# Kernel tuning notes

Measured on AMD Instinct MI355X. Metric: run time of the kernel, lower is better.

The kernel has to match this reference:

```python
import jax, jax.numpy as jnp
import numpy as np

N = 100000      # nodes
E = 1600000     # edges (before self-loops)
F_IN = 128      # dataset.num_features
H1 = 128        # hidden_channels/2
H2 = 256        # hidden_channels
C = 40          # dataset.num_classes
EPS = 1e-5      # BatchNorm eps
NEG_SLOPE = 0.2 # GATConv leaky_relu slope


def setup_inputs() -> dict:
    key = jax.random.key(0)
    ks = jax.random.split(key, 12)
    p = lambda k, shape: jax.random.normal(k, shape, jnp.float32) * 0.1
    x = jax.random.normal(ks[0], (N, F_IN), jnp.float32)
    edge_index = jax.random.randint(ks[1], (2, E), 0, N, dtype=jnp.int64)
    return dict(
        x=x, edge_index=edge_index,
        w1=p(ks[2], (F_IN, H1)), as1=p(ks[3], (H1,)), ad1=p(ks[4], (H1,)), b1=jnp.zeros(H1, jnp.float32),
        g1=jnp.ones(H1, jnp.float32), be1=jnp.zeros(H1, jnp.float32), rm1=jnp.zeros(H1, jnp.float32), rv1=jnp.ones(H1, jnp.float32),
        w2=p(ks[5], (H1, H2)), as2=p(ks[6], (H2,)), ad2=p(ks[7], (H2,)), b2=jnp.zeros(H2, jnp.float32),
        g2=jnp.ones(H2, jnp.float32), be2=jnp.zeros(H2, jnp.float32), rm2=jnp.zeros(H2, jnp.float32), rv2=jnp.ones(H2, jnp.float32),
        w3=p(ks[8], (H2, C)), as3=p(ks[9], (C,)), ad3=p(ks[10], (C,)), b3=jnp.zeros(C, jnp.float32),
    )


def gat_conv(x, src, dst, W, a_src, a_dst, b):
    """PyG GATConv (heads=1, add_self_loops already applied to src/dst)."""
    h = x @ W                                  # [N, F_out]
    alpha_src = h @ a_src                      # [N]
    alpha_dst = h @ a_dst                      # [N]
    logits = jax.nn.leaky_relu(alpha_src[src] + alpha_dst[dst], NEG_SLOPE)  # [E']
    # segment softmax over incoming edges of each dst node
    m = jax.ops.segment_max(logits, dst, num_segments=N)
    e = jnp.exp(logits - m[dst])
    denom = jax.ops.segment_sum(e, dst, num_segments=N)
    alpha = e / denom[dst]                     # [E']
    out = jax.ops.segment_sum(h[src] * alpha[:, None], dst, num_segments=N)
    return out + b


def bn_eval(x, gamma, beta, mean, var):
    return (x - mean) * jax.lax.rsqrt(var + EPS) * gamma + beta


def reference(x, edge_index,
              w1, as1, ad1, b1, g1, be1, rm1, rv1,
              w2, as2, ad2, b2, g2, be2, rm2, rv2,
              w3, as3, ad3, b3):
    # add self-loops once (PyG GATConv default add_self_loops=True)
    loop = jnp.arange(N, dtype=edge_index.dtype)
    src = jnp.concatenate([edge_index[0], loop])
    dst = jnp.concatenate([edge_index[1], loop])
    # eval mode: dropout is identity, BN uses running stats
    h = gat_conv(x, src, dst, w1, as1, ad1, b1)
    h = jnp.tanh(bn_eval(h, g1, be1, rm1, rv1))
    h = gat_conv(h, src, dst, w2, as2, ad2, b2)
    h = jnp.tanh(bn_eval(h, g2, be2, rm2, rv2))
    return gat_conv(h, src, dst, w3, as3, ad3, b3)
```

## Files before the change

### kernel.cpp

```cpp
#include <hip/hip_runtime.h>
#include <hip/hip_bf16.h>
#include <cstddef>

#define N_NODES 100000
#define E_EDGES 1600000
#define TOT_EDGES (E_EDGES + N_NODES)
#define NEG_SLOPE 0.2f
#define BN_EPS 1e-5f
#define NBKT ((N_NODES + 255) / 256)
#define NBA 512

typedef __attribute__((ext_vector_type(8))) short short8;
typedef __attribute__((ext_vector_type(4))) float f32x4;
typedef __attribute__((ext_vector_type(2))) float f32x2;
typedef __attribute__((ext_vector_type(4))) int int32x4;
typedef __attribute__((ext_vector_type(2))) int int32x2;

#if defined(__has_builtin)
#if __has_builtin(__builtin_amdgcn_make_buffer_rsrc) && __has_builtin(__builtin_amdgcn_raw_buffer_load_b128)
#define HAVE_BUFRSRC 1
#endif
#if __has_builtin(__builtin_amdgcn_make_buffer_rsrc) && __has_builtin(__builtin_amdgcn_raw_buffer_load_b64)
#define HAVE_BUF64 1
#endif
#endif

__device__ __forceinline__ unsigned short f2bf(float f) {
    union { float f; unsigned u; } c; c.f = f;
    unsigned u = c.u;
    u += 0x7fffu + ((u >> 16) & 1u);
    return (unsigned short)(u >> 16);
}
__device__ __forceinline__ float bf2f(unsigned short h) {
    union { unsigned u; float f; } c; c.u = ((unsigned)h) << 16;
    return c.f;
}
__device__ __forceinline__ unsigned short f2h(float f) {
    union { _Float16 h; unsigned short u; } c; c.h = (_Float16)f; return c.u;
}
__device__ __forceinline__ float lrelu(float t) {
    return (t > 0.f) ? t : NEG_SLOPE * t;
}
__device__ __forceinline__ float tanh_fast(float x) {
    float e = __expf(2.f * x);
    return 1.f - 2.f / (e + 1.f);
}
__device__ __forceinline__ unsigned short pk_fp8(float a, float b) {
    unsigned v;
    asm volatile("v_cvt_pk_fp8_f32 %0, %1, %2" : "=v"(v) : "v"(a), "v"(b));
    return (unsigned short)v;
}
__device__ __forceinline__ f32x2 unpk_fp8(unsigned u) {
    f32x2 r;
    asm volatile("v_cvt_pk_f32_fp8 %0, %1" : "=v"(r) : "v"(u));
    return r;
}

__device__ __forceinline__ float wave_sum63(float x) {
    x += __int_as_float(__builtin_amdgcn_update_dpp(0, __float_as_int(x), 0x111, 0xf, 0xf, true));
    x += __int_as_float(__builtin_amdgcn_update_dpp(0, __float_as_int(x), 0x112, 0xf, 0xf, true));
    x += __int_as_float(__builtin_amdgcn_update_dpp(0, __float_as_int(x), 0x114, 0xf, 0xf, true));
    x += __int_as_float(__builtin_amdgcn_update_dpp(0, __float_as_int(x), 0x118, 0xf, 0xf, true));
    x += __int_as_float(__builtin_amdgcn_update_dpp(0, __float_as_int(x), 0x142, 0xf, 0xf, true));
    x += __int_as_float(__builtin_amdgcn_update_dpp(0, __float_as_int(x), 0x143, 0xf, 0xf, true));
    return x;
}
__device__ __forceinline__ float wave_sum_bcast(float x) {
    return __int_as_float(__builtin_amdgcn_readlane(__float_as_int(wave_sum63(x)), 63));
}


__global__ __launch_bounds__(256) void csr_hist(const int* __restrict__ ei,
                                                int* __restrict__ bh) {
    __shared__ int h[NBKT];
    int t = threadIdx.x;
    for (int b = t; b < NBKT; b += 256) h[b] = 0;
    __syncthreads();
    int idx = blockIdx.x * 256 + t;
    const int stride = NBA * 256;
    for (int e = idx; e < TOT_EDGES; e += stride) {
        int d = (e < E_EDGES) ? ei[E_EDGES + e] : (e - E_EDGES);
        atomicAdd(&h[((unsigned)d) >> 8], 1);
    }
    __syncthreads();
    for (int b = t; b < NBKT; b += 256) bh[blockIdx.x * NBKT + b] = h[b];
}

__global__ __launch_bounds__(512) void csr_scan_blocks(int* __restrict__ bh,
                                                       int* __restrict__ totals) {
    __shared__ int s[NBA];
    int t = threadIdx.x, bin = blockIdx.x;
    int v = bh[t * NBKT + bin];
    s[t] = v;
    __syncthreads();
    for (int off = 1; off < NBA; off <<= 1) {
        int y = (t >= off) ? s[t - off] : 0;
        __syncthreads();
        s[t] += y;
        __syncthreads();
    }
    bh[t * NBKT + bin] = s[t] - v;
    if (t == NBA - 1) totals[bin] = s[t];
}

__global__ __launch_bounds__(512) void csr_scan_buckets(const int* __restrict__ totals,
                                                        int* __restrict__ starts) {
    __shared__ int s[512];
    int t = threadIdx.x;
    int v = (t < NBKT) ? totals[t] : 0;
    s[t] = v;
    __syncthreads();
    for (int off = 1; off < 512; off <<= 1) {
        int y = (t >= off) ? s[t - off] : 0;
        __syncthreads();
        s[t] += y;
        __syncthreads();
    }
    if (t < NBKT) starts[t] = s[t] - v;
    if (t == 0) starts[NBKT] = TOT_EDGES;
}

__global__ __launch_bounds__(256) void csr_scatter(const int* __restrict__ ei,
                                                   const int* __restrict__ bh,
                                                   const int* __restrict__ starts,
                                                   int* __restrict__ pairs) {
    __shared__ int wp[NBKT];
    int t = threadIdx.x;
    for (int b = t; b < NBKT; b += 256)
        wp[b] = starts[b] + bh[blockIdx.x * NBKT + b];
    __syncthreads();
    int idx = blockIdx.x * 256 + t;
    const int stride = NBA * 256;
    for (int e = idx; e < TOT_EDGES; e += stride) {
        int s, d;
        if (e < E_EDGES) { s = ei[e]; d = ei[E_EDGES + e]; }
        else             { s = e - E_EDGES; d = s; }
        int pos = atomicAdd(&wp[((unsigned)d) >> 8], 1);
        pairs[pos] = s | ((d & 255) << 20);
    }
}

__global__ __launch_bounds__(256) void csr_build(const int* __restrict__ pairs,
                                                 const int* __restrict__ starts,
                                                 int* __restrict__ row_ptr,
                                                 int* __restrict__ src_sorted) {
    __shared__ int nh[256];
    __shared__ int sc[256];
    __shared__ int wp[256];
    int k = blockIdx.x, t = threadIdx.x;
    int bs = starts[k], be = starts[k + 1];
    nh[t] = 0;
    __syncthreads();
    for (int i = bs + t; i < be; i += 256)
        atomicAdd(&nh[((unsigned)pairs[i]) >> 20], 1);
    __syncthreads();
    int v = nh[t];
    sc[t] = v;
    __syncthreads();
    for (int off = 1; off < 256; off <<= 1) {
        int y = (t >= off) ? sc[t - off] : 0;
        __syncthreads();
        sc[t] += y;
        __syncthreads();
    }
    int excl = sc[t] - v;
    int node = k * 256 + t;
    if (node <= N_NODES) row_ptr[node] = bs + excl;
    wp[t] = bs + excl;
    __syncthreads();
    for (int i = bs + t; i < be; i += 256) {
        unsigned p = (unsigned)pairs[i];
        int pos = atomicAdd(&wp[p >> 20], 1);
        src_sorted[pos] = (int)(p & 0xFFFFFu);
    }
}

__global__ __launch_bounds__(256) void wprep_all(
    const float* __restrict__ w1, const float* __restrict__ w2, const float* __restrict__ w3,
    const float* __restrict__ as1, const float* __restrict__ ad1,
    const float* __restrict__ as2, const float* __restrict__ ad2,
    const float* __restrict__ as3, const float* __restrict__ ad3,
    unsigned short* __restrict__ w1th, unsigned short* __restrict__ w1tl,
    unsigned short* __restrict__ w2th, unsigned short* __restrict__ w2tl,
    unsigned short* __restrict__ w3th, unsigned short* __restrict__ w3tl,
    unsigned short* __restrict__ ab1h, unsigned short* __restrict__ ab1l,
    unsigned short* __restrict__ ab3h, unsigned short* __restrict__ ab3l,
    float* __restrict__ ws2f, float* __restrict__ wd2f) {
    const int T1 = 128 * 128, T2 = 256 * 128, T3 = 48 * 256;
    const int W = T1 + T2 + T3;
    int idx = blockIdx.x * 256 + threadIdx.x;
    if (idx < W) {
        float v; unsigned short* th; unsigned short* tl; int o;
        if (idx < T1) {
            int n = idx / 128, k = idx % 128;
            v = w1[k * 128 + n]; th = w1th; tl = w1tl; o = idx;
        } else if (idx < T1 + T2) {
            int i = idx - T1; int n = i / 128, k = i % 128;
            v = w2[k * 256 + n]; th = w2th; tl = w2tl; o = i;
        } else {
            int i = idx - T1 - T2; int n = i / 256, k = i % 256;
            v = (n < 40) ? w3[k * 40 + n] : 0.f; th = w3th; tl = w3tl; o = i;
        }
        unsigned short h = f2bf(v);
        th[o] = h;
        tl[o] = f2bf(v - bf2f(h));
        return;
    }
    int j = idx - W;
    if (j < 2048) {
        int r = j / 128, k = j % 128;
        float v = 0.f;
        if (r < 2) {
            const float* a = r ? ad1 : as1;
            const float* wr = w1 + (size_t)k * 128;
            for (int n = 0; n < 128; n++) v += wr[n] * a[n];
        }
        unsigned short h = f2bf(v);
        ab1h[j] = h; ab1l[j] = f2bf(v - bf2f(h));
    } else if (j < 2048 + 4096) {
        int i = j - 2048; int r = i / 256, k = i % 256;
        float v = 0.f;
        if (r < 2) {
            const float* a = r ? ad3 : as3;
            const float* wr = w3 + (size_t)k * 40;
            for (int n = 0; n < 40; n++) v += wr[n] * a[n];
        }
        unsigned short h = f2bf(v);
        ab3h[i] = h; ab3l[i] = f2bf(v - bf2f(h));
    } else if (j < 2048 + 4096 + 256) {
        int i = j - 2048 - 4096; int r = i / 128, k = i % 128;
        const float* a = r ? ad2 : as2;
        const float* wr = w2 + (size_t)k * 256;
        float v = 0.f;
        for (int n = 0; n < 256; n++) v += wr[n] * a[n];
        if (r == 0) ws2f[k] = v; else wd2f[k] = v;
    }
}

template<int K, int NTILES, int MWAVES, int NWAVES, int NACT, bool ASPLIT, bool ALPHA, bool BNT, bool CFRAG, bool CHALF, bool AF32>
__global__ __launch_bounds__(256) void mfma_gemm(
    const unsigned short* __restrict__ Ahi, const unsigned short* __restrict__ Alo,
    const unsigned short* __restrict__ BThi, const unsigned short* __restrict__ BTlo,
    const unsigned short* __restrict__ ABh, const unsigned short* __restrict__ ABl,
    unsigned short* __restrict__ Chi, int ldc,
    const float* __restrict__ bias, const float* __restrict__ gamma,
    const float* __restrict__ beta, const float* __restrict__ rmean,
    const float* __restrict__ rvar,
    float* __restrict__ asrc, float* __restrict__ adst, int M)
{
    int lane = threadIdx.x & 63;
    int wave = threadIdx.x >> 6;
    int quad = lane >> 4;
    int l16  = lane & 15;
    long mbase = (long)blockIdx.x * (64 * MWAVES) + (long)(wave / NWAVES) * 64;
    int n0 = ((wave % NWAVES) + blockIdx.y * NWAVES) * (NTILES * 16);
    bool aw = ((wave % NWAVES) == 0) && (blockIdx.y == 0);
    const size_t CSTRIDE = (size_t)M * 32;

    size_t roff[4];
#pragma unroll
    for (int i = 0; i < 4; i++) {
        long r = mbase + i * 16 + l16;
        if (r > M - 1) r = M - 1;
        roff[i] = AF32 ? ((size_t)r * K + (size_t)(quad * 8))
                       : ((size_t)r * 32 + (size_t)(quad * 8));
    }
    const unsigned short* bh[NTILES]; const unsigned short* bl[NTILES];
#pragma unroll
    for (int j = 0; j < NTILES; j++) {
        long n = n0 + j * 16 + l16;
        bh[j] = BThi + n * K; bl[j] = BTlo + n * K;
    }
    const unsigned short* bah = nullptr; const unsigned short* bal = nullptr;
    if constexpr (ALPHA) { bah = ABh + (size_t)l16 * K; bal = ABl + (size_t)l16 * K; }
    const int ko = quad * 8;

    f32x4 acc[4][NTILES];
    f32x4 acca[4];
#pragma unroll
    for (int i = 0; i < 4; i++) {
        acca[i] = (f32x4){0.f, 0.f, 0.f, 0.f};
#pragma unroll
        for (int j = 0; j < NTILES; j++)
            acc[i][j] = (f32x4){0.f, 0.f, 0.f, 0.f};
    }

    for (int kc = 0; kc < K / 32; kc++) {
        const int k0 = kc * 32;
        short8 vah[4], vall[4], vbh[NTILES], vbl[NTILES];
#pragma unroll
        for (int i = 0; i < 4; i++) {
            if constexpr (AF32) {
                const float* xf = (const float*)Ahi;
                const float* pa = xf + roff[i] + kc * 32;
                f32x4 va = *(const f32x4*)pa;
                f32x4 vb = *(const f32x4*)(pa + 4);
#pragma unroll
                for (int q = 0; q < 8; q++) {
                    float v = (q < 4) ? va[q] : vb[q - 4];
                    unsigned short h = f2bf(v);
                    vah[i][q] = (short)h;
                    vall[i][q] = (short)f2bf(v - bf2f(h));
                }
            } else {
                const unsigned short* Ah = Ahi + (size_t)kc * CSTRIDE;
                vah[i] = *(const short8*)(Ah + roff[i]);
                if constexpr (ASPLIT) {
                    const unsigned short* Al = Alo + (size_t)kc * CSTRIDE;
                    vall[i] = *(const short8*)(Al + roff[i]);
                }
            }
        }
#pragma unroll
        for (int j = 0; j < NTILES; j++) {
            vbh[j] = *(const short8*)(bh[j] + k0 + ko);
            vbl[j] = *(const short8*)(bl[j] + k0 + ko);
        }
#pragma unroll
        for (int i = 0; i < 4; i++)
#pragma unroll
            for (int j = 0; j < NTILES; j++) {
                acc[i][j] = __builtin_amdgcn_mfma_f32_16x16x32_bf16(vah[i], vbh[j], acc[i][j], 0, 0, 0);
                acc[i][j] = __builtin_amdgcn_mfma_f32_16x16x32_bf16(vah[i], vbl[j], acc[i][j], 0, 0, 0);
                if constexpr (ASPLIT)
                    acc[i][j] = __builtin_amdgcn_mfma_f32_16x16x32_bf16(vall[i], vbh[j], acc[i][j], 0, 0, 0);
            }
        if constexpr (ALPHA) {
            if (aw) {
                short8 vbah = *(const short8*)(bah + k0 + ko);
                short8 vbal = *(const short8*)(bal + k0 + ko);
#pragma unroll
                for (int i = 0; i < 4; i++) {
                    acca[i] = __builtin_amdgcn_mfma_f32_16x16x32_bf16(vah[i], vbah, acca[i], 0, 0, 0);
                    acca[i] = __builtin_amdgcn_mfma_f32_16x16x32_bf16(vah[i], vbal, acca[i], 0, 0, 0);
                    if constexpr (ASPLIT)
                        acca[i] = __builtin_amdgcn_mfma_f32_16x16x32_bf16(vall[i], vbah, acca[i], 0, 0, 0);
                }
            }
        }
    }

#pragma unroll
    for (int i = 0; i < 4; i++)
#pragma unroll
        for (int j = 0; j < NTILES; j++) {
            int col = n0 + j * 16 + l16;
            float bb = 0.f, rs = 1.f, gg = 1.f, bt = 0.f, rm = 0.f;
            if constexpr (BNT) {
                bb = bias[col]; gg = gamma[col]; bt = beta[col];
                rm = rmean[col]; rs = rsqrtf(rvar[col] + BN_EPS);
            }
#pragma unroll
            for (int r = 0; r < 4; r++) {
                long row = mbase + i * 16 + quad * 4 + r;
                if (row < M && col < NACT) {
                    float v = acc[i][j][r];
                    if constexpr (BNT) v = tanh_fast((v + bb - rm) * rs * gg + bt);
                    if constexpr (CFRAG) {
                        Chi[(size_t)(col >> 5) * CSTRIDE + (size_t)row * 32 + (col & 31)] = f2bf(v);
                    } else {
                        Chi[row * ldc + col] = CHALF ? f2h(v) : f2bf(v);
                    }
                }
            }
        }
    if constexpr (ALPHA) {
        if (aw) {
#pragma unroll
            for (int i = 0; i < 4; i++)
#pragma unroll
                for (int r = 0; r < 4; r++) {
                    long row = mbase + i * 16 + quad * 4 + r;
                    if (row < M) {
                        float v = acca[i][r];
                        if (l16 == 0) asrc[row] = v;
                        else if (l16 == 1) adst[row] = v;
                    }
                }
        }
    }
}

template<int MODE>
__global__ __launch_bounds__(256) void gat_agg_wide(
    const unsigned short* __restrict__ hsrc,
    const float* __restrict__ asrc, const float* __restrict__ adst,
    const int* __restrict__ row_ptr, const int* __restrict__ src_sorted,
    const float* __restrict__ bias, const float* __restrict__ gamma,
    const float* __restrict__ beta, const float* __restrict__ rmean,
    const float* __restrict__ rvar,
    const float* __restrict__ wsn, const float* __restrict__ wdn,
    unsigned short* __restrict__ ohi,
    float* __restrict__ outf,
    float* __restrict__ asrc_n, float* __restrict__ adst_n)
{
    constexpr int SH  = (MODE == 0) ? 8 : 7;
    constexpr int BPL = (MODE == 0) ? 16 : 8;
    constexpr int NF  = (MODE == 2) ? 4 : 8;

    __shared__ __align__(16) float2 esw[4][64];
    __shared__ __align__(16) float red[4][4][132];

    int wave = threadIdx.x >> 6;
    int lane = threadIdx.x & 63;
    int node = blockIdx.x * 4 + wave;
    if (node >= N_NODES) return;

    int start = row_ptr[node];
    int end = row_ptr[node + 1];
    int deg = end - start;
    float ad = adst[node];
    int sub = lane >> 4;
    int foff = (lane & 15) * BPL;
    int tpos = (lane & 3) * 16 + (lane >> 2);

#if defined(HAVE_BUFRSRC) && defined(HAVE_BUF64)
    auto rsrc = __builtin_amdgcn_make_buffer_rsrc((void*)hsrc, (short)0,
                                                  N_NODES << SH, 0x00020000);
#endif

    float acc[NF];
#pragma unroll
    for (int i = 0; i < NF; i++) acc[i] = 0.f;

    auto ld = [&](int vo) {
        if constexpr (MODE == 0) {
#if defined(HAVE_BUFRSRC) && defined(HAVE_BUF64)
            return __builtin_amdgcn_raw_buffer_load_b128(rsrc, vo, 0, 0);
#else
            return *reinterpret_cast<const int32x4*>(
                reinterpret_cast<const char*>(hsrc) + (unsigned)vo);
#endif
        } else {
#if defined(HAVE_BUFRSRC) && defined(HAVE_BUF64)
            return __builtin_amdgcn_raw_buffer_load_b64(rsrc, vo, 0, 0);
#else
            return *reinterpret_cast<const int32x2*>(
                reinterpret_cast<const char*>(hsrc) + (unsigned)vo);
#endif
        }
    };
    auto fmaN = [&](auto u, float ww) {
        if constexpr (MODE == 0) {
            union { decltype(u) v; unsigned w[4]; } c; c.v = u;
#pragma unroll
            for (int i = 0; i < 4; i++) {
                union { unsigned u; _Float16 h[2]; } t; t.u = c.w[i];
                acc[2 * i]     += ww * (float)t.h[0];
                acc[2 * i + 1] += ww * (float)t.h[1];
            }
        } else if constexpr (MODE == 1) {
            union { decltype(u) v; unsigned w[2]; } c; c.v = u;
#pragma unroll
            for (int i = 0; i < 2; i++) {
                f32x2 lo = unpk_fp8(c.w[i]);
                f32x2 hi = unpk_fp8(c.w[i] >> 16);
                acc[4 * i]     += ww * lo.x;
                acc[4 * i + 1] += ww * lo.y;
                acc[4 * i + 2] += ww * hi.x;
                acc[4 * i + 3] += ww * hi.y;
            }
        } else {
            union { decltype(u) v; unsigned w[2]; } c; c.v = u;
#pragma unroll
            for (int i = 0; i < 2; i++) {
                union { unsigned u; _Float16 h[2]; } t; t.u = c.w[i];
                acc[2 * i]     += ww * (float)t.h[0];
                acc[2 * i + 1] += ww * (float)t.h[1];
            }
        }
    };
    auto gather = [&](int nst) {
        const float2* ep = &esw[wave][sub * 16];
#pragma unroll
        for (int b = 0; b < 4; b++) {
            int s0 = b * 4;
            if (s0 < nst) {
                f32x4 p01 = *(const f32x4*)(ep + s0);
                f32x4 p23 = *(const f32x4*)(ep + s0 + 2);
                bool g1 = s0 + 1 < nst, g2 = s0 + 2 < nst, g3 = s0 + 3 < nst;
                auto u0 = ld(__float_as_int(p01.x) + foff);
                decltype(u0) u1, u2, u3;
                if (g1) u1 = ld(__float_as_int(p01.z) + foff);
                if (g2) u2 = ld(__float_as_int(p23.x) + foff);
                if (g3) u3 = ld(__float_as_int(p23.z) + foff);
                fmaN(u0, p01.y);
                if (g1) fmaN(u1, p01.w);
                if (g2) fmaN(u2, p23.y);
                if (g3) fmaN(u3, p23.w);
            }
        }
    };

    if (deg <= 64) {
        int e = start + lane;
        int s = 0; float w = 0.f;
        if (e < end) { s = src_sorted[e]; w = __expf(lrelu(asrc[s] + ad)); }
        float dsum = wave_sum_bcast(w);
        esw[wave][tpos] = make_float2(__int_as_float(s << SH), w * (1.0f / dsum));
        gather((deg + 3) >> 2);
    } else {
        float part = 0.f;
        for (int cs = start; cs < end; cs += 64) {
            int e = cs + lane;
            if (e < end) part += __expf(lrelu(asrc[src_sorted[e]] + ad));
        }
        float inv = 1.0f / wave_sum_bcast(part);
        for (int cs = start; cs < end; cs += 64) {
            int e = cs + lane;
            int s = 0; float w = 0.f;
            if (e < end) { s = src_sorted[e]; w = __expf(lrelu(asrc[s] + ad)) * inv; }
            esw[wave][tpos] = make_float2(__int_as_float(s << SH), w);
            gather((min(64, end - cs) + 3) >> 2);
        }
    }

    if constexpr (MODE == 2) {
        *reinterpret_cast<f32x4*>(&red[wave][sub][(lane & 15) * 4]) =
            (f32x4){acc[0], acc[1], acc[2], acc[3]};
        float t = 0.f;
#pragma unroll
        for (int g = 0; g < 4; g++) t += red[wave][g][lane];
        if (lane < 40) outf[(size_t)node * 40 + lane] = t + bias[lane];
    } else {
        f32x4* dst = reinterpret_cast<f32x4*>(&red[wave][sub][(lane & 15) * 8]);
        dst[0] = (f32x4){acc[0], acc[1], acc[2], acc[3]};
        dst[1] = (f32x4){acc[4], acc[5], acc[6], acc[7]};
        f32x2 tsum = (f32x2){0.f, 0.f};
#pragma unroll
        for (int g = 0; g < 4; g++)
            tsum += *reinterpret_cast<const f32x2*>(&red[wave][g][lane * 2]);

        if constexpr (MODE == 0) {
            float vals[2];
#pragma unroll
            for (int v = 0; v < 2; v++) {
                int f = lane * 2 + v;
                float val = tsum[v] + bias[f];
                float rs = rsqrtf(rvar[f] + BN_EPS);
                vals[v] = tanh_fast((val - rmean[f]) * rs * gamma[f] + beta[f]);
            }
            ohi[(size_t)node * 64 + lane] = pk_fp8(vals[0], vals[1]);
            float ps = vals[0] * wsn[lane * 2] + vals[1] * wsn[lane * 2 + 1];
            float pd = vals[0] * wdn[lane * 2] + vals[1] * wdn[lane * 2 + 1];
            ps = wave_sum63(ps);
            pd = wave_sum63(pd);
            if (lane == 63) { asrc_n[node] = ps; adst_n[node] = pd; }
        } else {
            const size_t CSTRIDE = (size_t)N_NODES * 32;
            unsigned w0 = (unsigned)f2bf(tsum[0]) | ((unsigned)f2bf(tsum[1]) << 16);
            size_t a = (size_t)(lane >> 4) * CSTRIDE + (size_t)node * 32 + ((lane * 2) & 31);
            *reinterpret_cast<unsigned*>(ohi + a) = w0;
        }
    }
}


static inline size_t align256(size_t x) { return (x + 255) & ~(size_t)255; }

extern "C" void kernel_launch(void* const* d_in, const int* in_sizes, int n_in,
                              void* d_out, int out_size, void* d_ws, size_t ws_size,
                              hipStream_t stream) {
    const float* x   = (const float*)d_in[0];
    const int* ei    = (const int*)d_in[1];
    const float* w1  = (const float*)d_in[2];
    const float* as1 = (const float*)d_in[3];
    const float* ad1 = (const float*)d_in[4];
    const float* b1  = (const float*)d_in[5];
    const float* g1  = (const float*)d_in[6];
    const float* be1 = (const float*)d_in[7];
    const float* rm1 = (const float*)d_in[8];
    const float* rv1 = (const float*)d_in[9];
    const float* w2  = (const float*)d_in[10];
    const float* as2 = (const float*)d_in[11];
    const float* ad2 = (const float*)d_in[12];
    const float* b2  = (const float*)d_in[13];
    const float* g2  = (const float*)d_in[14];
    const float* be2 = (const float*)d_in[15];
    const float* rm2 = (const float*)d_in[16];
    const float* rv2 = (const float*)d_in[17];
    const float* w3  = (const float*)d_in[18];
    const float* as3 = (const float*)d_in[19];
    const float* ad3 = (const float*)d_in[20];
    const float* b3  = (const float*)d_in[21];
    float* out = (float*)d_out;

    const size_t P128 = align256((size_t)N_NODES * 128 * 2);
    const size_t P256 = align256((size_t)N_NODES * 256 * 2);

    char* p = (char*)d_ws;
    char* regA = p; p += P256;
    char* regB = p; p += P256;
    unsigned short* o1p  = (unsigned short*)regA;
    unsigned short* o2hi = (unsigned short*)regA;
    unsigned short* h1h  = (unsigned short*)regB;
    unsigned short* g2hi = (unsigned short*)regB;
    unsigned short* h3h  = (unsigned short*)regB;
    int* pairs  = (int*)regB;
    int* bhist  = (int*)(regB + align256((size_t)TOT_EDGES * 4));
    int* totals = (int*)((char*)bhist + align256((size_t)NBA * NBKT * 4));
    int* starts = (int*)((char*)totals + align256((size_t)NBKT * 4));

    float* asrcA = (float*)p; p += align256((size_t)N_NODES * 4);
    float* adstA = (float*)p; p += align256((size_t)N_NODES * 4);
    float* asrcB = (float*)p; p += align256((size_t)N_NODES * 4);
    float* adstB = (float*)p; p += align256((size_t)N_NODES * 4);
    int* row_ptr   = (int*)p; p += align256((size_t)(N_NODES + 1) * 4);
    int* src_sorted = (int*)p; p += align256((size_t)TOT_EDGES * 4);
    unsigned short* w1th = (unsigned short*)p; p += align256(128 * 128 * 2);
    unsigned short* w1tl = (unsigned short*)p; p += align256(128 * 128 * 2);
    unsigned short* w2th = (unsigned short*)p; p += align256(256 * 128 * 2);
    unsigned short* w2tl = (unsigned short*)p; p += align256(256 * 128 * 2);
    unsigned short* w3th = (unsigned short*)p; p += align256(48 * 256 * 2);
    unsigned short* w3tl = (unsigned short*)p; p += align256(48 * 256 * 2);
    unsigned short* ab1h = (unsigned short*)p; p += align256(16 * 128 * 2);
    unsigned short* ab1l = (unsigned short*)p; p += align256(16 * 128 * 2);
    unsigned short* ab3h = (unsigned short*)p; p += align256(16 * 256 * 2);
    unsigned short* ab3l = (unsigned short*)p; p += align256(16 * 256 * 2);
    float* ws2f = (float*)p; p += align256(128 * 4);
    float* wd2f = (float*)p; p += align256(128 * 4);

    const int WTOT = 128 * 128 + 256 * 128 + 48 * 256 + 2048 + 4096 + 256;

    wprep_all<<<(WTOT + 255) / 256, 256, 0, stream>>>(
        w1, w2, w3, as1, ad1, as2, ad2, as3, ad3,
        w1th, w1tl, w2th, w2tl, w3th, w3tl,
        ab1h, ab1l, ab3h, ab3l, ws2f, wd2f);

    csr_hist<<<NBA, 256, 0, stream>>>(ei, bhist);
    csr_scan_blocks<<<NBKT, 512, 0, stream>>>(bhist, totals);
    csr_scan_buckets<<<1, 512, 0, stream>>>(totals, starts);
    csr_scatter<<<NBA, 256, 0, stream>>>(ei, bhist, starts, pairs);
    csr_build<<<NBKT, 256, 0, stream>>>(pairs, starts, row_ptr, src_sorted);

    const int NWB = (N_NODES + 3) / 4;
    const int G64 = (N_NODES + 63) / 64;
    const int G256 = (N_NODES + 255) / 256;

    mfma_gemm<128, 2, 1, 4, 128, true, true, false, false, true, true><<<G64, 256, 0, stream>>>(
        (const unsigned short*)x, nullptr, w1th, w1tl, ab1h, ab1l, h1h, 128,
        nullptr, nullptr, nullptr, nullptr, nullptr, asrcA, adstA, N_NODES);
    gat_agg_wide<0><<<NWB, 256, 0, stream>>>(
        h1h, asrcA, adstA, row_ptr, src_sorted,
        b1, g1, be1, rm1, rv1, ws2f, wd2f,
        o1p, nullptr, asrcB, adstB);

    gat_agg_wide<1><<<NWB, 256, 0, stream>>>(
        o1p, asrcB, adstB, row_ptr, src_sorted,
        nullptr, nullptr, nullptr, nullptr, nullptr, nullptr, nullptr,
        g2hi, nullptr, nullptr, nullptr);
    mfma_gemm<128, 4, 1, 4, 256, false, false, true, true, false, false><<<G64, 256, 0, stream>>>(
        g2hi, nullptr, w2th, w2tl, nullptr, nullptr, o2hi, 256,
        b2, g2, be2, rm2, rv2, nullptr, nullptr, N_NODES);

    mfma_gemm<256, 3, 4, 1, 48, false, true, false, false, true, false><<<G256, 256, 0, stream>>>(
        o2hi, nullptr, w3th, w3tl, ab3h, ab3l, h3h, 64,
        nullptr, nullptr, nullptr, nullptr, nullptr, asrcA, adstA, N_NODES);
    gat_agg_wide<2><<<NWB, 256, 0, stream>>>(
        h3h, asrcA, adstA, row_ptr, src_sorted,
        b3, nullptr, nullptr, nullptr, nullptr, nullptr, nullptr,
        nullptr, out, nullptr, nullptr);
}
```

Measured before the change: 461.2 us.

## Fuse layer-2 GEMM with BN/tanh and layer-3 GEMM via shared memory

Merges the layer-2 transform GEMM (with bias, batch-norm and tanh epilogue) and the layer-3 GEMM plus attention-score projection into one kernel. The 256-wide intermediate stays in LDS per 64-row tile instead of being written to and re-read from global memory. This drops one launch and about 100 MB of bf16 global traffic. In exchange, each block uses 40 KB of LDS, which limits occupancy, and the layer-3 stage runs with only one 16-row tile per wave.

```diff
diff --git a/kernel.cpp b/kernel.cpp
--- a/kernel.cpp
+++ b/kernel.cpp
@@ -377,6 +377,141 @@
                         else if (l16 == 1) adst[row] = v;
                     }
                 }
+        }
+    }
+}
+
+__global__ __launch_bounds__(256) void gemm23_fused(
+    const unsigned short* __restrict__ Ahi,
+    const unsigned short* __restrict__ B2h, const unsigned short* __restrict__ B2l,
+    const float* __restrict__ bias, const float* __restrict__ gamma,
+    const float* __restrict__ beta, const float* __restrict__ rmean,
+    const float* __restrict__ rvar,
+    const unsigned short* __restrict__ B3h, const unsigned short* __restrict__ B3l,
+    const unsigned short* __restrict__ AB3h, const unsigned short* __restrict__ AB3l,
+    unsigned short* __restrict__ h3,
+    float* __restrict__ asrc, float* __restrict__ adst, int M)
+{
+    constexpr int LW = 40;
+    __shared__ unsigned short o2l[8 * 64 * LW];
+
+    int lane = threadIdx.x & 63;
+    int wave = threadIdx.x >> 6;
+    int quad = lane >> 4;
+    int l16  = lane & 15;
+    long mbase = (long)blockIdx.x * 64;
+    const size_t CSTRIDE = (size_t)M * 32;
+    const int ko = quad * 8;
+
+    size_t roff[4];
+#pragma unroll
+    for (int i = 0; i < 4; i++) {
+        long r = mbase + i * 16 + l16;
+        if (r > M - 1) r = M - 1;
+        roff[i] = (size_t)r * 32 + (size_t)ko;
+    }
+    int n0 = wave * 64;
+    const unsigned short* bh[4]; const unsigned short* bl[4];
+#pragma unroll
+    for (int j = 0; j < 4; j++) {
+        long n = n0 + j * 16 + l16;
+        bh[j] = B2h + n * 128; bl[j] = B2l + n * 128;
+    }
+
+    f32x4 acc[4][4];
+#pragma unroll
+    for (int i = 0; i < 4; i++)
+#pragma unroll
+        for (int j = 0; j < 4; j++)
+            acc[i][j] = (f32x4){0.f, 0.f, 0.f, 0.f};
+
+    for (int kc = 0; kc < 4; kc++) {
+        const int k0 = kc * 32;
+        const unsigned short* Ah = Ahi + (size_t)kc * CSTRIDE;
+        short8 vah[4], vbh[4], vbl[4];
+#pragma unroll
+        for (int i = 0; i < 4; i++) vah[i] = *(const short8*)(Ah + roff[i]);
+#pragma unroll
+        for (int j = 0; j < 4; j++) {
+            vbh[j] = *(const short8*)(bh[j] + k0 + ko);
+            vbl[j] = *(const short8*)(bl[j] + k0 + ko);
+        }
+#pragma unroll
+        for (int i = 0; i < 4; i++)
+#pragma unroll
+            for (int j = 0; j < 4; j++) {
+                acc[i][j] = __builtin_amdgcn_mfma_f32_16x16x32_bf16(vah[i], vbh[j], acc[i][j], 0, 0, 0);
+                acc[i][j] = __builtin_amdgcn_mfma_f32_16x16x32_bf16(vah[i], vbl[j], acc[i][j], 0, 0, 0);
+            }
+    }
+
+#pragma unroll
+    for (int j = 0; j < 4; j++) {
+        int col = n0 + j * 16 + l16;
+        float bb = bias[col], gg = gamma[col], bt = beta[col];
+        float rm = rmean[col], rs = rsqrtf(rvar[col] + BN_EPS);
+        int cbase = (col >> 5) * 64 * LW + (col & 31);
+#pragma unroll
+        for (int i = 0; i < 4; i++)
+#pragma unroll
+            for (int r = 0; r < 4; r++) {
+                int li = i * 16 + quad * 4 + r;
+                float v = tanh_fast((acc[i][j][r] + bb - rm) * rs * gg + bt);
+                o2l[cbase + li * LW] = f2bf(v);
+            }
+    }
+    __syncthreads();
+
+    const unsigned short* b3h[3]; const unsigned short* b3l[3];
+#pragma unroll
+    for (int j = 0; j < 3; j++) {
+        long n = j * 16 + l16;
+        b3h[j] = B3h + n * 256; b3l[j] = B3l + n * 256;
+    }
+    const unsigned short* bah = AB3h + (size_t)l16 * 256;
+    const unsigned short* bal = AB3l + (size_t)l16 * 256;
+    int lrow = wave * 16 + l16;
+
+    f32x4 acc3[3], acca;
+#pragma unroll
+    for (int j = 0; j < 3; j++) acc3[j] = (f32x4){0.f, 0.f, 0.f, 0.f};
+    acca = (f32x4){0.f, 0.f, 0.f, 0.f};
+
+    for (int kc = 0; kc < 8; kc++) {
+        const int k0 = kc * 32;
+        short8 a = *(const short8*)(o2l + (kc * 64 + lrow) * LW + ko);
+        short8 vbh[3], vbl[3];
+#pragma unroll
+        for (int j = 0; j < 3; j++) {
+            vbh[j] = *(const short8*)(b3h[j] + k0 + ko);
+            vbl[j] = *(const short8*)(b3l[j] + k0 + ko);
+        }
+#pragma unroll
+        for (int j = 0; j < 3; j++) {
+            acc3[j] = __builtin_amdgcn_mfma_f32_16x16x32_bf16(a, vbh[j], acc3[j], 0, 0, 0);
+            acc3[j] = __builtin_amdgcn_mfma_f32_16x16x32_bf16(a, vbl[j], acc3[j], 0, 0, 0);
+        }
+        short8 vbah = *(const short8*)(bah + k0 + ko);
+        short8 vbal = *(const short8*)(bal + k0 + ko);
+        acca = __builtin_amdgcn_mfma_f32_16x16x32_bf16(a, vbah, acca, 0, 0, 0);
+        acca = __builtin_amdgcn_mfma_f32_16x16x32_bf16(a, vbal, acca, 0, 0, 0);
+    }
+
+#pragma unroll
+    for (int j = 0; j < 3; j++) {
+        int col = j * 16 + l16;
+#pragma unroll
+        for (int r = 0; r < 4; r++) {
+            long row = mbase + wave * 16 + quad * 4 + r;
+            if (row < M) h3[(size_t)row * 64 + col] = f2h(acc3[j][r]);
+        }
+    }
+#pragma unroll
+    for (int r = 0; r < 4; r++) {
+        long row = mbase + wave * 16 + quad * 4 + r;
+        if (row < M) {
+            if (l16 == 0) asrc[row] = acca[r];
+            else if (l16 == 1) adst[row] = acca[r];
         }
     }
 }
@@ -592,10 +727,9 @@
     char* regA = p; p += P256;
     char* regB = p; p += P256;
     unsigned short* o1p  = (unsigned short*)regA;
-    unsigned short* o2hi = (unsigned short*)regA;
+    unsigned short* h3h  = (unsigned short*)regA;
     unsigned short* h1h  = (unsigned short*)regB;
     unsigned short* g2hi = (unsigned short*)regB;
-    unsigned short* h3h  = (unsigned short*)regB;
     int* pairs  = (int*)regB;
     int* bhist  = (int*)(regB + align256((size_t)TOT_EDGES * 4));
     int* totals = (int*)((char*)bhist + align256((size_t)NBA * NBKT * 4));
@@ -635,7 +769,6 @@
 
     const int NWB = (N_NODES + 3) / 4;
     const int G64 = (N_NODES + 63) / 64;
-    const int G256 = (N_NODES + 255) / 256;
 
     mfma_gemm<128, 2, 1, 4, 128, true, true, false, false, true, true><<<G64, 256, 0, stream>>>(
         (const unsigned short*)x, nullptr, w1th, w1tl, ab1h, ab1l, h1h, 128,
@@ -649,13 +782,11 @@
         o1p, asrcB, adstB, row_ptr, src_sorted,
         nullptr, nullptr, nullptr, nullptr, nullptr, nullptr, nullptr,
         g2hi, nullptr, nullptr, nullptr);
-    mfma_gemm<128, 4, 1, 4, 256, false, false, true, true, false, false><<<G64, 256, 0, stream>>>(
-        g2hi, nullptr, w2th, w2tl, nullptr, nullptr, o2hi, 256,
-        b2, g2, be2, rm2, rv2, nullptr, nullptr, N_NODES);
-
-    mfma_gemm<256, 3, 4, 1, 48, false, true, false, false, true, false><<<G256, 256, 0, stream>>>(
-        o2hi, nullptr, w3th, w3tl, ab3h, ab3l, h3h, 64,
-        nullptr, nullptr, nullptr, nullptr, nullptr, asrcA, adstA, N_NODES);
+
+    gemm23_fused<<<G64, 256, 0, stream>>>(
+        g2hi, w2th, w2tl, b2, g2, be2, rm2, rv2,
+        w3th, w3tl, ab3h, ab3l, h3h, asrcA, adstA, N_NODES);
+
     gat_agg_wide<2><<<NWB, 256, 0, stream>>>(
         h3h, asrcA, adstA, row_ptr, src_sorted,
         b3, nullptr, nullptr, nullptr, nullptr, nullptr, nullptr,
```

Result: no change. 463.4 us (+0.5%).
